# Performance work log

Measured on AMD Instinct MI355X. Metric: run time of the kernel, lower is better.

## Reference

```python
import jax, jax.numpy as jnp
import numpy as np

ALPHA = 0.2          # LeakyReLU negative slope
NEG_INF = -9e15      # mask value used by the original module

def setup_inputs() -> dict:
    key = jax.random.key(0)
    k1, k2, k3, k4 = jax.random.split(key, 4)
    B, N, F_in, F_out = 8, 2048, 128, 64
    h = jax.random.normal(k1, (B, N, F_in), dtype=jnp.float32)
    # dense 0/1 adjacency with self-loops so every softmax row is valid
    adj = jax.random.randint(k2, (B, N, N), 0, 2).astype(jnp.float32)
    adj = jnp.maximum(adj, jnp.eye(N, dtype=jnp.float32)[None])
    # xavier_uniform with gain=1.414 (as in torch init)
    gain = 1.414
    limW = gain * np.sqrt(6.0 / (F_in + F_out))
    W = jax.random.uniform(k3, (F_in, F_out), jnp.float32, -limW, limW)
    lima = gain * np.sqrt(6.0 / (2 * F_out + 1))
    attention_w = jax.random.uniform(k4, (2 * F_out, 1), jnp.float32, -lima, lima)
    return {"h": h, "adj": adj, "W": W, "attention_w": attention_w}

def reference(h, adj, W, attention_w):
    # hidden: (B, N, F_out)
    hidden = jnp.matmul(h, W)
    F_out = W.shape[1]
    # Decompose additive attention: e[b,i,j] = leakyrelu(Wh_i . a1 + Wh_j . a2)
    # (mathematically identical to the concat + matmul in the original, but
    # avoids materializing the (B,N,N,2F) tensor)
    a1 = attention_w[:F_out, 0]   # (F_out,)
    a2 = attention_w[F_out:, 0]   # (F_out,)
    s1 = jnp.einsum('bnf,f->bn', hidden, a1)  # (B, N)
    s2 = jnp.einsum('bnf,f->bn', hidden, a2)  # (B, N)
    e = s1[:, :, None] + s2[:, None, :]       # (B, N, N)
    e = jnp.where(e >= 0, e, ALPHA * e)       # LeakyReLU
    scores = jnp.where(adj > 0, e * adj, NEG_INF)
    attention = jax.nn.softmax(scores, axis=2)
    # dropout is identity at inference (training=False)
    h_prime = jnp.matmul(attention, hidden)   # (B, N, F_out)
    return jax.nn.elu(h_prime)                # concat=True -> ELU
```

## Files before the change

kernel.cpp:

```cpp
#include <hip/hip_runtime.h>
#include <stdint.h>

typedef float f32x4 __attribute__((ext_vector_type(4)));
typedef uint32_t u32x4 __attribute__((ext_vector_type(4)));
typedef short s16x8 __attribute__((ext_vector_type(8)));

#define BB   8
#define NN   2048
#define FIN  128
#define FOUT 64

__device__ __forceinline__ uint32_t cvt_pk_bf16(float lo, float hi) {
  uint32_t r;
  asm("v_cvt_pk_bf16_f32 %0, %1, %2" : "=v"(r) : "v"(lo), "v"(hi));
  return r;
}

__device__ __forceinline__ s16x8 mk_s16x8(uint32_t a, uint32_t b, uint32_t c, uint32_t d) {
  union { uint32_t u[4]; s16x8 v; } x;
  x.u[0] = a; x.u[1] = b; x.u[2] = c; x.u[3] = d;
  return x.v;
}

__global__ void k1_hidden(const float* __restrict__ h, const float* __restrict__ W,
                          const float* __restrict__ attw, ushort* __restrict__ hidT,
                          float* __restrict__ s1, float* __restrict__ s2) {
  __shared__ ushort wlds[FOUT * 136];
  const int tid = threadIdx.x;

  for (int idx = tid; idx < FIN * FOUT; idx += 256) {
    int k = idx >> 6, c = idx & 63;
    wlds[c * 136 + k] = (ushort)(cvt_pk_bf16(W[idx], 0.f) & 0xffffu);
  }
  __syncthreads();

  const int bid = ((blockIdx.x & 7) << 5) | (blockIdx.x >> 3);
  const int lane = tid & 63, wid = tid >> 6;
  const int q = lane & 15, g = lane >> 4;
  const int wrow0 = bid * 64 + wid * 16;
  const int b  = wrow0 >> 11;
  const int n0 = wrow0 & (NN - 1);

  const float* hrow = h + (size_t)(wrow0 + q) * FIN + 8 * g;

  f32x4 acc[4];
  #pragma unroll
  for (int nt = 0; nt < 4; ++nt) acc[nt] = {0.f, 0.f, 0.f, 0.f};

  #pragma unroll
  for (int kk = 0; kk < 4; ++kk) {
    f32x4 h0 = *(const f32x4*)(hrow + 32 * kk);
    f32x4 h1 = *(const f32x4*)(hrow + 32 * kk + 4);
    s16x8 A = mk_s16x8(cvt_pk_bf16(h0[0], h0[1]), cvt_pk_bf16(h0[2], h0[3]),
                       cvt_pk_bf16(h1[0], h1[1]), cvt_pk_bf16(h1[2], h1[3]));
    #pragma unroll
    for (int nt = 0; nt < 4; ++nt) {
      s16x8 Bf = *(const s16x8*)(&wlds[(nt * 16 + q) * 136 + 32 * kk + 8 * g]);
      acc[nt] = __builtin_amdgcn_mfma_f32_16x16x32_bf16(A, Bf, acc[nt], 0, 0, 0);
    }
  }

  float a1v[4], a2v[4];
  #pragma unroll
  for (int nt = 0; nt < 4; ++nt) {
    a1v[nt] = attw[nt * 16 + q];
    a2v[nt] = attw[64 + nt * 16 + q];
  }
  float p1[4], p2[4];
  #pragma unroll
  for (int r = 0; r < 4; ++r) {
    float v1 = 0.f, v2 = 0.f;
    #pragma unroll
    for (int nt = 0; nt < 4; ++nt) { v1 += acc[nt][r] * a1v[nt]; v2 += acc[nt][r] * a2v[nt]; }
    #pragma unroll
    for (int m = 1; m < 16; m <<= 1) { v1 += __shfl_xor(v1, m, 64); v2 += __shfl_xor(v2, m, 64); }
    p1[r] = v1; p2[r] = v2;
  }
  if (q < 4) {
    int gr = wrow0 + 4 * g + q;
    float v1 = (q == 0) ? p1[0] : (q == 1) ? p1[1] : (q == 2) ? p1[2] : p1[3];
    float v2 = (q == 0) ? p2[0] : (q == 1) ? p2[1] : (q == 2) ? p2[2] : p2[3];
    s1[gr] = v1; s2[gr] = v2;
  }

  #pragma unroll
  for (int nt = 0; nt < 4; ++nt) {
    uint32_t lo = cvt_pk_bf16(acc[nt][0], acc[nt][1]);
    uint32_t hi = cvt_pk_bf16(acc[nt][2], acc[nt][3]);
    *(uint2*)(hidT + ((size_t)b * FOUT + nt * 16 + q) * NN + n0 + 4 * g) = make_uint2(lo, hi);
  }
}

__global__ __launch_bounds__(512, 4) void kF(
    const float* __restrict__ adj, const ushort* __restrict__ hidT,
    const float* __restrict__ s1g, const float* __restrict__ s2g,
    float* __restrict__ out) {
  __shared__ __align__(16) char smem[74240];
  float* s2l   = (float*)(smem + 65536);
  float* partl = (float*)(smem + 73728);

  const int tid = threadIdx.x;
  const int sb = ((blockIdx.x & 7) << 6) | (blockIdx.x >> 3);
  const int b  = sb >> 6;
  const int i0 = (sb & 63) << 5;

  const int lane = tid & 63, wid = tid >> 6;
  const int q = lane & 15, g = lane >> 4;
  const int rg = wid >> 2, jw = wid & 3;

  *(f32x4*)(s2l + tid * 4) = *(const f32x4*)(s2g + b * NN + tid * 4);
  const float s1r = s1g[b * NN + i0 + rg * 16 + q];

  const float* adjB = adj + ((size_t)(b * NN + i0 + wid)) * NN + lane * 4;
  const int f0 = tid >> 5, sl = tid & 31;
  const ushort* hBp = hidT + ((size_t)(b * FOUT + f0)) * NN + sl * 8;
  const int aswz = (lane << 4), awx = (wid & 7) << 4;
  const int hswz = (sl << 4) ^ ((f0 & 7) << 4);

  f32x4 aA, aB, aC, aD; u32x4 hA, hB, hC, hD;

#define ADJ_LOAD(cc) do {                                                     \
    const float* p_ = adjB + (cc) * 256;                                      \
    aA = *(const f32x4*)(p_);                                                 \
    aB = *(const f32x4*)(p_ + (size_t) 8 * NN);                               \
    aC = *(const f32x4*)(p_ + (size_t)16 * NN);                               \
    aD = *(const f32x4*)(p_ + (size_t)24 * NN);                               \
  } while (0)

#define ADJ_WRITE() do {                                                      \
    *(f32x4*)(smem + (wid     ) * 1024 + (aswz ^ awx)) = aA;                  \
    *(f32x4*)(smem + (wid +  8) * 1024 + (aswz ^ awx)) = aB;                  \
    *(f32x4*)(smem + (wid + 16) * 1024 + (aswz ^ awx)) = aC;                  \
    *(f32x4*)(smem + (wid + 24) * 1024 + (aswz ^ awx)) = aD;                  \
  } while (0)

#define H_LOAD(cc) do {                                                       \
    const ushort* p_ = hBp + (cc) * 256;                                      \
    hA = *(const u32x4*)(p_);                                                 \
    hB = *(const u32x4*)(p_ + (size_t)16 * NN);                               \
    hC = *(const u32x4*)(p_ + (size_t)32 * NN);                               \
    hD = *(const u32x4*)(p_ + (size_t)48 * NN);                               \
  } while (0)

#define H_WRITE() do {                                                        \
    char* d_ = smem + 32768;                                                  \
    *(u32x4*)(d_ + (f0     ) * 512 + hswz) = hA;                              \
    *(u32x4*)(d_ + (f0 + 16) * 512 + hswz) = hB;                              \
    *(u32x4*)(d_ + (f0 + 32) * 512 + hswz) = hC;                              \
    *(u32x4*)(d_ + (f0 + 48) * 512 + hswz) = hD;                              \
  } while (0)

  ADJ_LOAD(0); H_LOAD(0);
  ADJ_WRITE(); H_WRITE();

  f32x4 acc0 = {0,0,0,0}, acc1 = {0,0,0,0}, acc2 = {0,0,0,0}, acc3 = {0,0,0,0};
  float lsum = 0.f;
  const int xr = (q & 7) << 4;
  const int arow = (rg * 16 + q) * 1024;

  #pragma unroll
  for (int c = 0; c < 8; ++c) {
    __syncthreads();
    if (c < 7) { ADJ_LOAD(c + 1); H_LOAD(c + 1); }

    #pragma unroll
    for (int s = 0; s < 2; ++s) {
      const int joff = jw * 256 + s * 128 + g * 32;
      f32x4 av0 = *(const f32x4*)(smem + arow + ((joff     ) ^ xr));
      f32x4 av1 = *(const f32x4*)(smem + arow + ((joff + 16) ^ xr));
      const int jl = jw * 64 + s * 32 + 8 * g;
      f32x4 t0 = *(const f32x4*)(s2l + c * 256 + jl);
      f32x4 t1 = *(const f32x4*)(s2l + c * 256 + jl + 4);
      const int hoff = (jw * 128 + s * 64 + g * 16) ^ xr;
      const char* hL = smem + 32768;
      u32x4 b0 = *(const u32x4*)(hL + (( 0 + q) << 9) + hoff);
      u32x4 b1 = *(const u32x4*)(hL + ((16 + q) << 9) + hoff);
      u32x4 b2 = *(const u32x4*)(hL + ((32 + q) << 9) + hoff);
      u32x4 b3 = *(const u32x4*)(hL + ((48 + q) << 9) + hoff);

      float e0 = s1r + t0[0], e1 = s1r + t0[1], e2 = s1r + t0[2], e3 = s1r + t0[3];
      float e4 = s1r + t1[0], e5 = s1r + t1[1], e6 = s1r + t1[2], e7 = s1r + t1[3];
      float p0 = av0[0] * __expf(fmaxf(e0, 0.2f * e0));
      float p1 = av0[1] * __expf(fmaxf(e1, 0.2f * e1));
      float p2 = av0[2] * __expf(fmaxf(e2, 0.2f * e2));
      float p3 = av0[3] * __expf(fmaxf(e3, 0.2f * e3));
      float p4 = av1[0] * __expf(fmaxf(e4, 0.2f * e4));
      float p5 = av1[1] * __expf(fmaxf(e5, 0.2f * e5));
      float p6 = av1[2] * __expf(fmaxf(e6, 0.2f * e6));
      float p7 = av1[3] * __expf(fmaxf(e7, 0.2f * e7));
      lsum += ((p0 + p1) + (p2 + p3)) + ((p4 + p5) + (p6 + p7));

      s16x8 A = mk_s16x8(cvt_pk_bf16(p0, p1), cvt_pk_bf16(p2, p3),
                         cvt_pk_bf16(p4, p5), cvt_pk_bf16(p6, p7));
      union { u32x4 u; s16x8 v; } w0, w1, w2, w3;
      w0.u = b0; w1.u = b1; w2.u = b2; w3.u = b3;
      acc0 = __builtin_amdgcn_mfma_f32_16x16x32_bf16(A, w0.v, acc0, 0, 0, 0);
      acc1 = __builtin_amdgcn_mfma_f32_16x16x32_bf16(A, w1.v, acc1, 0, 0, 0);
      acc2 = __builtin_amdgcn_mfma_f32_16x16x32_bf16(A, w2.v, acc2, 0, 0, 0);
      acc3 = __builtin_amdgcn_mfma_f32_16x16x32_bf16(A, w3.v, acc3, 0, 0, 0);
    }

    __syncthreads();
    if (c < 7) { ADJ_WRITE(); H_WRITE(); }
  }

  lsum += __shfl_xor(lsum, 16, 64);
  lsum += __shfl_xor(lsum, 32, 64);
  if (lane < 16) partl[jw * 32 + rg * 16 + lane] = lsum;

  float* part = (float*)smem;
  #pragma unroll
  for (int r = 0; r < 4; ++r) {
    const int il = rg * 16 + 4 * g + r;
    part[(jw * 32 + il) * 64 +  0 + q] = acc0[r];
    part[(jw * 32 + il) * 64 + 16 + q] = acc1[r];
    part[(jw * 32 + il) * 64 + 32 + q] = acc2[r];
    part[(jw * 32 + il) * 64 + 48 + q] = acc3[r];
  }
  __syncthreads();

  #pragma unroll
  for (int k = 0; k < 4; ++k) {
    const int idx = tid + 512 * k;
    const int row = idx >> 6, col = idx & 63;
    float v  = (part[(0 * 32 + row) * 64 + col] + part[(1 * 32 + row) * 64 + col]) +
               (part[(2 * 32 + row) * 64 + col] + part[(3 * 32 + row) * 64 + col]);
    float li = (partl[0 * 32 + row] + partl[1 * 32 + row]) +
               (partl[2 * 32 + row] + partl[3 * 32 + row]);
    float hp = v / li;
    out[(size_t)(b * NN + i0 + row) * 64 + col] = (hp > 0.f) ? hp : expm1f(hp);
  }
}

extern "C" void kernel_launch(void* const* d_in, const int* in_sizes, int n_in,
                              void* d_out, int out_size, void* d_ws, size_t ws_size,
                              hipStream_t stream) {
  const float* h    = (const float*)d_in[0];
  const float* adj  = (const float*)d_in[1];
  const float* W    = (const float*)d_in[2];
  const float* attw = (const float*)d_in[3];
  float* out = (float*)d_out;

  char* ws = (char*)d_ws;
  ushort* hidT = (ushort*)ws;
  float*  s1   = (float*)(ws + (2u << 20));
  float*  s2   = (float*)(ws + (2u << 20) + (64u << 10));

  hipLaunchKernelGGL(k1_hidden, dim3(256), dim3(256), 0, stream, h, W, attw, hidT, s1, s2);
  hipLaunchKernelGGL(kF, dim3(512), dim3(512), 0, stream, adj, hidT, s1, s2, out);
}
```

Measured before the change: 41.95 us.

## Pack adjacency tile into byte mask in LDS and raise occupancy bound

The adjacency chunk staged in shared memory is converted at store time from fp32 values to one byte per entry, with a new XOR swizzle. The softmax numerator becomes a select on the mask byte instead of a multiply by the adjacency value. This shrinks the LDS footprint from about 74 KB to about 49 KB, cuts LDS write and read traffic, and lets the launch bound rise to 6 so more blocks can fit per CU. It relies on adjacency being 0/1, which the previous multiply form already assumed, and the higher launch bound may tighten the register budget.

```diff
diff --git a/kernel.cpp b/kernel.cpp
--- a/kernel.cpp
+++ b/kernel.cpp
@@ -91,13 +91,13 @@
   }
 }
 
-__global__ __launch_bounds__(512, 4) void kF(
+__global__ __launch_bounds__(512, 6) void kF(
     const float* __restrict__ adj, const ushort* __restrict__ hidT,
     const float* __restrict__ s1g, const float* __restrict__ s2g,
     float* __restrict__ out) {
-  __shared__ __align__(16) char smem[74240];
-  float* s2l   = (float*)(smem + 65536);
-  float* partl = (float*)(smem + 73728);
+  __shared__ __align__(16) char smem[49664];
+  float* s2l   = (float*)(smem + 40960);
+  float* partl = (float*)(smem + 49152);
 
   const int tid = threadIdx.x;
   const int sb = ((blockIdx.x & 7) << 6) | (blockIdx.x >> 3);
@@ -114,7 +114,7 @@
   const float* adjB = adj + ((size_t)(b * NN + i0 + wid)) * NN + lane * 4;
   const int f0 = tid >> 5, sl = tid & 31;
   const ushort* hBp = hidT + ((size_t)(b * FOUT + f0)) * NN + sl * 8;
-  const int aswz = (lane << 4), awx = (wid & 7) << 4;
+  const int awoff = (4 * lane) ^ ((wid & 7) << 3);
   const int hswz = (sl << 4) ^ ((f0 & 7) << 4);
 
   f32x4 aA, aB, aC, aD; u32x4 hA, hB, hC, hD;
@@ -127,11 +127,14 @@
     aD = *(const f32x4*)(p_ + (size_t)24 * NN);                               \
   } while (0)
 
+#define PK8(v) ((v[0] > 0.f ? 1u : 0u) | (v[1] > 0.f ? 0x100u : 0u) |         \
+                (v[2] > 0.f ? 0x10000u : 0u) | (v[3] > 0.f ? 0x1000000u : 0u))
+
 #define ADJ_WRITE() do {                                                      \
-    *(f32x4*)(smem + (wid     ) * 1024 + (aswz ^ awx)) = aA;                  \
-    *(f32x4*)(smem + (wid +  8) * 1024 + (aswz ^ awx)) = aB;                  \
-    *(f32x4*)(smem + (wid + 16) * 1024 + (aswz ^ awx)) = aC;                  \
-    *(f32x4*)(smem + (wid + 24) * 1024 + (aswz ^ awx)) = aD;                  \
+    *(uint32_t*)(smem + (wid     ) * 256 + awoff) = PK8(aA);                  \
+    *(uint32_t*)(smem + (wid +  8) * 256 + awoff) = PK8(aB);                  \
+    *(uint32_t*)(smem + (wid + 16) * 256 + awoff) = PK8(aC);                  \
+    *(uint32_t*)(smem + (wid + 24) * 256 + awoff) = PK8(aD);                  \
   } while (0)
 
 #define H_LOAD(cc) do {                                                       \
@@ -143,7 +146,7 @@
   } while (0)
 
 #define H_WRITE() do {                                                        \
-    char* d_ = smem + 32768;                                                  \
+    char* d_ = smem + 8192;                                                   \
     *(u32x4*)(d_ + (f0     ) * 512 + hswz) = hA;                              \
     *(u32x4*)(d_ + (f0 + 16) * 512 + hswz) = hB;                              \
     *(u32x4*)(d_ + (f0 + 32) * 512 + hswz) = hC;                              \
@@ -156,7 +159,8 @@
   f32x4 acc0 = {0,0,0,0}, acc1 = {0,0,0,0}, acc2 = {0,0,0,0}, acc3 = {0,0,0,0};
   float lsum = 0.f;
   const int xr = (q & 7) << 4;
-  const int arow = (rg * 16 + q) * 1024;
+  const int arow = (rg * 16 + q);
+  const int aswz = (arow & 7) << 3;
 
   #pragma unroll
   for (int c = 0; c < 8; ++c) {
@@ -165,14 +169,12 @@
 
     #pragma unroll
     for (int s = 0; s < 2; ++s) {
-      const int joff = jw * 256 + s * 128 + g * 32;
-      f32x4 av0 = *(const f32x4*)(smem + arow + ((joff     ) ^ xr));
-      f32x4 av1 = *(const f32x4*)(smem + arow + ((joff + 16) ^ xr));
       const int jl = jw * 64 + s * 32 + 8 * g;
+      uint2 am = *(const uint2*)(smem + arow * 256 + ((jl) ^ aswz));
       f32x4 t0 = *(const f32x4*)(s2l + c * 256 + jl);
       f32x4 t1 = *(const f32x4*)(s2l + c * 256 + jl + 4);
       const int hoff = (jw * 128 + s * 64 + g * 16) ^ xr;
-      const char* hL = smem + 32768;
+      const char* hL = smem + 8192;
       u32x4 b0 = *(const u32x4*)(hL + (( 0 + q) << 9) + hoff);
       u32x4 b1 = *(const u32x4*)(hL + ((16 + q) << 9) + hoff);
       u32x4 b2 = *(const u32x4*)(hL + ((32 + q) << 9) + hoff);
@@ -180,14 +182,14 @@
 
       float e0 = s1r + t0[0], e1 = s1r + t0[1], e2 = s1r + t0[2], e3 = s1r + t0[3];
       float e4 = s1r + t1[0], e5 = s1r + t1[1], e6 = s1r + t1[2], e7 = s1r + t1[3];
-      float p0 = av0[0] * __expf(fmaxf(e0, 0.2f * e0));
-      float p1 = av0[1] * __expf(fmaxf(e1, 0.2f * e1));
-      float p2 = av0[2] * __expf(fmaxf(e2, 0.2f * e2));
-      float p3 = av0[3] * __expf(fmaxf(e3, 0.2f * e3));
-      float p4 = av1[0] * __expf(fmaxf(e4, 0.2f * e4));
-      float p5 = av1[1] * __expf(fmaxf(e5, 0.2f * e5));
-      float p6 = av1[2] * __expf(fmaxf(e6, 0.2f * e6));
-      float p7 = av1[3] * __expf(fmaxf(e7, 0.2f * e7));
+      float p0 = (am.x & 0x000000ffu) ? __expf(fmaxf(e0, 0.2f * e0)) : 0.f;
+      float p1 = (am.x & 0x0000ff00u) ? __expf(fmaxf(e1, 0.2f * e1)) : 0.f;
+      float p2 = (am.x & 0x00ff0000u) ? __expf(fmaxf(e2, 0.2f * e2)) : 0.f;
+      float p3 = (am.x & 0xff000000u) ? __expf(fmaxf(e3, 0.2f * e3)) : 0.f;
+      float p4 = (am.y & 0x000000ffu) ? __expf(fmaxf(e4, 0.2f * e4)) : 0.f;
+      float p5 = (am.y & 0x0000ff00u) ? __expf(fmaxf(e5, 0.2f * e5)) : 0.f;
+      float p6 = (am.y & 0x00ff0000u) ? __expf(fmaxf(e6, 0.2f * e6)) : 0.f;
+      float p7 = (am.y & 0xff000000u) ? __expf(fmaxf(e7, 0.2f * e7)) : 0.f;
       lsum += ((p0 + p1) + (p2 + p3)) + ((p4 + p5) + (p6 + p7));
 
       s16x8 A = mk_s16x8(cvt_pk_bf16(p0, p1), cvt_pk_bf16(p2, p3),
@@ -208,7 +210,7 @@
   lsum += __shfl_xor(lsum, 32, 64);
   if (lane < 16) partl[jw * 32 + rg * 16 + lane] = lsum;
 
-  float* part = (float*)smem;
+  float* part = (float*)(smem + 8192);
   #pragma unroll
   for (int r = 0; r < 4; ++r) {
     const int il = rg * 16 + 4 * g + r;
```

After: 115.1 us. 2.74x slower.
